# Kernel tuning notes

Measured on AMD Instinct MI355X. Metric: run time of the kernel, lower is better.

Reference implementation:

```python
import jax, jax.numpy as jnp
import numpy as np

KERNEL_MUL = 2.0
KERNEL_NUM = 5


def setup_inputs() -> dict:
    key = jax.random.key(0)
    k1, k2 = jax.random.split(key)
    N, D = 4096, 256
    source = jax.random.normal(k1, (N, D), dtype=jnp.float32)
    target = jax.random.normal(k2, (N, D), dtype=jnp.float32)
    return {"source": source, "target": target}


def _gaussian_kernel_sum(source, target):
    # total: [2N, D]
    total = jnp.concatenate([source, target], axis=0)
    n = total.shape[0]
    sq = jnp.sum(total * total, axis=1)  # [2N]
    L2 = sq[:, None] + sq[None, :] - 2.0 * (total @ total.T)  # [2N, 2N]
    # Bandwidth from detached mean of off-diagonal-normalized sum (torch uses .data)
    bandwidth = jax.lax.stop_gradient(jnp.sum(L2)) / (n * n - n)
    bandwidth = bandwidth / (KERNEL_MUL ** (KERNEL_NUM // 2))
    kernels = sum(
        jnp.exp(-L2 / (bandwidth * (KERNEL_MUL ** i))) for i in range(KERNEL_NUM)
    )
    return kernels


def reference(source, target):
    b = source.shape[0]
    K = _gaussian_kernel_sum(source, target)
    XX = jnp.mean(K[:b, :b])
    YY = jnp.mean(K[b:, b:])
    XY = jnp.mean(K[:b, b:])
    YX = jnp.mean(K[b:, :b])
    return XX + YY - XY - YX
```

## Files before the change

kernel.cpp:

```cpp
#include <hip/hip_runtime.h>


#define NROWS 8192
#define HALF  4096
#define DIM   256
#define CONVB 256
#define NTILE 2080

typedef __bf16 bf16x8 __attribute__((ext_vector_type(8)));
typedef float f32x4 __attribute__((ext_vector_type(4)));
typedef unsigned short ushort8 __attribute__((ext_vector_type(8)));

__device__ __forceinline__ const float* row_ptr(const float* src, const float* tgt, int r) {
    return (r < HALF) ? (src + (size_t)r * DIM) : (tgt + (size_t)(r - HALF) * DIM);
}

__device__ __forceinline__ unsigned short bf16_rne(float x) {
    unsigned int u = __builtin_bit_cast(unsigned int, x);
    return (unsigned short)((u + 0x7FFFu + ((u >> 16) & 1u)) >> 16);
}

__global__ __launch_bounds__(256) void k_conv(const float* __restrict__ src,
                                              const float* __restrict__ tgt,
                                              unsigned short* __restrict__ hi,
                                              float* __restrict__ sq,
                                              float* __restrict__ part,
                                              double* __restrict__ parts1,
                                              float* __restrict__ out) {
    __shared__ __align__(16) unsigned short sh_hi[32 * 32 * 8];
    __shared__ float4 cs[4][64];
    __shared__ double s1s[4];

    int w = threadIdx.x >> 6, lane = threadIdx.x & 63;
    int r0 = blockIdx.x * 32;
    int g  = lane >> 1, j = lane & 1;

    float4 v[8];
    #pragma unroll
    for (int i = 0; i < 8; ++i) {
        int row = r0 + w * 8 + i;
        v[i] = ((const float4*)row_ptr(src, tgt, row))[lane];
    }

    float4 csum = {0.f, 0.f, 0.f, 0.f};
    double s1w = 0.0;
    #pragma unroll
    for (int i = 0; i < 8; ++i) {
        int rl  = w * 8 + i;
        float xs[4] = {v[i].x, v[i].y, v[i].z, v[i].w};
        unsigned short hs[4];
        #pragma unroll
        for (int k = 0; k < 4; ++k) hs[k] = bf16_rne(xs[k]);
        ushort4 h4 = {hs[0], hs[1], hs[2], hs[3]};
        int so = (g * 32 + rl) * 8 + j * 4;
        *(ushort4*)&sh_hi[so] = h4;
        csum.x += xs[0]; csum.y += xs[1]; csum.z += xs[2]; csum.w += xs[3];
        float s = xs[0] * xs[0] + xs[1] * xs[1] + xs[2] * xs[2] + xs[3] * xs[3];
        #pragma unroll
        for (int off = 32; off; off >>= 1) s += __shfl_xor(s, off, 64);
        if (lane == 0) { sq[r0 + rl] = s; s1w += (double)s; }
    }
    __syncthreads();
    int panel = blockIdx.x >> 2, quarter = blockIdx.x & 3;
    #pragma unroll
    for (int c = threadIdx.x; c < 1024; c += 256) {
        int gg = c >> 5, r = c & 31;
        size_t goff = (((size_t)panel * 32 + gg) * 128 + quarter * 32 + r) * 8;
        *(ushort8*)&hi[goff] = *(const ushort8*)&sh_hi[c * 8];
    }
    cs[w][lane] = csum;
    if (lane == 0) s1s[w] = s1w;
    __syncthreads();
    if (w == 0) {
        float4 a = cs[0][lane], b = cs[1][lane], c = cs[2][lane], d = cs[3][lane];
        float4 tot = {a.x + b.x + c.x + d.x, a.y + b.y + c.y + d.y,
                      a.z + b.z + c.z + d.z, a.w + b.w + c.w + d.w};
        *(float4*)&part[(size_t)blockIdx.x * DIM + lane * 4] = tot;
        if (lane == 0) parts1[blockIdx.x] = s1s[0] + s1s[1] + s1s[2] + s1s[3];
    }
    if (blockIdx.x == 0 && threadIdx.x == 0) out[0] = 0.0f;
}

__global__ __launch_bounds__(256) void k_scale(const double* __restrict__ parts1,
                                               const float* __restrict__ part,
                                               float* __restrict__ scale) {
    __shared__ double sh[256];
    int t = threadIdx.x;
    sh[t] = parts1[t];
    __syncthreads();
    for (int off = 128; off; off >>= 1) {
        if (t < off) sh[t] += sh[t + off];
        __syncthreads();
    }
    double S1 = sh[0];
    __syncthreads();
    float c0 = 0.f, c1 = 0.f, c2 = 0.f, c3 = 0.f;
    #pragma unroll 16
    for (int b = 0; b < CONVB; b += 4) {
        c0 += part[(b + 0) * DIM + t];
        c1 += part[(b + 1) * DIM + t];
        c2 += part[(b + 2) * DIM + t];
        c3 += part[(b + 3) * DIM + t];
    }
    double c = (double)((c0 + c1) + (c2 + c3));
    sh[t] = c * c;
    __syncthreads();
    for (int off = 128; off; off >>= 1) {
        if (t < off) sh[t] += sh[t + off];
        __syncthreads();
    }
    if (t == 0) {
        double S2    = sh[0];
        double n     = (double)NROWS;
        double sumL2 = 2.0 * n * S1 - 2.0 * S2;
        double bw    = sumL2 / (n * n - n) / 4.0;
        *scale = (float)(-1.0 / (16.0 * bw * 0.69314718055994530942));
    }
}

__global__ __launch_bounds__(256, 2) void k_pairs(const unsigned short* __restrict__ hi,
                                                  const float* __restrict__ sq,
                                                  const float* __restrict__ scale_p,
                                                  float* __restrict__ out) {
    int id = blockIdx.x;
    int I = 0;
    for (;;) {
        int cnt = 64 - I;
        if (id < cnt) break;
        id -= cnt; ++I;
    }
    int J = I + id;

    __shared__ float wsum[4];

    int t    = threadIdx.x;
    int lane = t & 63;
    int w    = t >> 6;
    int lr   = lane & 15, lq = lane >> 4;
    int wr   = w >> 1, wc = w & 1;

    float wgt = (J == I) ? 1.0f : 2.0f;
    float sgn = ((I < 32) == (J < 32)) ? 1.0f : -1.0f;

    size_t aBase = (size_t)I * 4096 + (size_t)lq * 128 + wr * 64 + lr;
    size_t bBase = (size_t)J * 4096 + (size_t)lq * 128 + wc * 64 + lr;
    const ushort8* pAh = (const ushort8*)hi + aBase;
    const ushort8* pBh = (const ushort8*)hi + bBase;

    f32x4 acc[4][4];
    #pragma unroll
    for (int m = 0; m < 4; ++m)
        #pragma unroll
        for (int n = 0; n < 4; ++n) acc[m][n] = (f32x4){0.f, 0.f, 0.f, 0.f};

    bf16x8 aH[2][4], bH[2][4];
    #pragma unroll
    for (int m = 0; m < 4; ++m) aH[0][m] = __builtin_bit_cast(bf16x8, pAh[m * 16]);
    #pragma unroll
    for (int n = 0; n < 4; ++n) bH[0][n] = __builtin_bit_cast(bf16x8, pBh[n * 16]);

    #pragma unroll
    for (int it = 0; it < DIM / 32; ++it) {
        int cur = it & 1, nxt = cur ^ 1;
        if (it < DIM / 32 - 1) {
            #pragma unroll
            for (int m = 0; m < 4; ++m)
                aH[nxt][m] = __builtin_bit_cast(bf16x8, pAh[(it + 1) * 512 + m * 16]);
            #pragma unroll
            for (int n = 0; n < 4; ++n)
                bH[nxt][n] = __builtin_bit_cast(bf16x8, pBh[(it + 1) * 512 + n * 16]);
        }
        #pragma unroll
        for (int m = 0; m < 4; ++m)
            #pragma unroll
            for (int n = 0; n < 4; ++n)
                acc[m][n] = __builtin_amdgcn_mfma_f32_16x16x32_bf16(aH[cur][m], bH[cur][n], acc[m][n], 0, 0, 0);
    }

    float scale = *scale_p;
    int ro_eff = I * 128 + wr * 64;
    int co_eff = J * 128 + wc * 64;
    float4 sqa4[4];
    float  sqbv[4];
    #pragma unroll
    for (int m = 0; m < 4; ++m) sqa4[m] = *(const float4*)&sq[ro_eff + m * 16 + lq * 4];
    #pragma unroll
    for (int n = 0; n < 4; ++n) sqbv[n] = sq[co_eff + n * 16 + lr];

    float tsum = 0.0f;
    #pragma unroll
    for (int m = 0; m < 4; ++m) {
        float sa[4] = {sqa4[m].x, sqa4[m].y, sqa4[m].z, sqa4[m].w};
        #pragma unroll
        for (int n = 0; n < 4; ++n) {
            #pragma unroll
            for (int r = 0; r < 4; ++r) {
                float L2  = sa[r] + sqbv[n] - 2.0f * acc[m][n][r];
                float u   = __builtin_amdgcn_exp2f(scale * L2);
                float u2  = u * u;
                float u4  = u2 * u2;
                float u8  = u4 * u4;
                float u16 = u8 * u8;
                tsum += u + u2 + u4 + u8 + u16;
            }
        }
    }

    #pragma unroll
    for (int off = 32; off; off >>= 1) tsum += __shfl_xor(tsum, off, 64);
    if (lane == 0) wsum[w] = tsum;
    __syncthreads();
    if (t == 0) {
        float tot = wsum[0] + wsum[1] + wsum[2] + wsum[3];
        atomicAdd(out, tot * sgn * wgt * (1.0f / ((float)HALF * (float)HALF)));
    }
}

extern "C" void kernel_launch(void* const* d_in, const int* in_sizes, int n_in,
                              void* d_out, int out_size, void* d_ws, size_t ws_size,
                              hipStream_t stream) {
    const float* src = (const float*)d_in[0];
    const float* tgt = (const float*)d_in[1];
    float* out = (float*)d_out;

    char* ws = (char*)d_ws;
    float*  scale  = (float*)(ws + 16);
    float*  sq     = (float*)(ws + 64);
    float*  part   = (float*)(ws + 64 + 32768);
    double* parts1 = (double*)(ws + 64 + 32768 + 262144);
    unsigned short* hi = (unsigned short*)(ws + 297024);

    k_conv <<<CONVB, 256, 0, stream>>>(src, tgt, hi, sq, part, parts1, out);
    k_scale<<<1, 256, 0, stream>>>(parts1, part, scale);
    k_pairs<<<NTILE, 256, 0, stream>>>(hi, sq, scale, out);
}
```

Before: 111.0 us.

## Switch Gram matrix computation from bf16 to fp8 MFMA with fp8-consistent norms

Operands are now quantized to fp8 (e4m3) instead of bf16, and the pairwise dot products use the fp8 16x16x32 MFMA. Row squared norms used in the L2 formula are computed from the dequantized fp8 values so that the diagonal stays near zero, while the bandwidth statistic still uses exact fp32 norms. The packed layout is reorganised into 16-byte chunks holding two k-slices, and all operand fragments are loaded up front instead of double-buffered. This halves the operand bytes read per tile and uses a higher-throughput MFMA, at the cost of a large precision loss in the dot products that may push the result outside tolerance.

```diff
diff --git a/kernel.cpp b/kernel.cpp
--- a/kernel.cpp
+++ b/kernel.cpp
@@ -7,33 +7,25 @@
 #define CONVB 256
 #define NTILE 2080
 
-typedef __bf16 bf16x8 __attribute__((ext_vector_type(8)));
 typedef float f32x4 __attribute__((ext_vector_type(4)));
-typedef unsigned short ushort8 __attribute__((ext_vector_type(8)));
 
 __device__ __forceinline__ const float* row_ptr(const float* src, const float* tgt, int r) {
     return (r < HALF) ? (src + (size_t)r * DIM) : (tgt + (size_t)(r - HALF) * DIM);
 }
 
-__device__ __forceinline__ unsigned short bf16_rne(float x) {
-    unsigned int u = __builtin_bit_cast(unsigned int, x);
-    return (unsigned short)((u + 0x7FFFu + ((u >> 16) & 1u)) >> 16);
-}
-
 __global__ __launch_bounds__(256) void k_conv(const float* __restrict__ src,
                                               const float* __restrict__ tgt,
-                                              unsigned short* __restrict__ hi,
+                                              unsigned char* __restrict__ hi,
                                               float* __restrict__ sq,
                                               float* __restrict__ part,
                                               double* __restrict__ parts1,
                                               float* __restrict__ out) {
-    __shared__ __align__(16) unsigned short sh_hi[32 * 32 * 8];
+    __shared__ __align__(16) unsigned char sh8[32 * 256];
     __shared__ float4 cs[4][64];
     __shared__ double s1s[4];
 
     int w = threadIdx.x >> 6, lane = threadIdx.x & 63;
     int r0 = blockIdx.x * 32;
-    int g  = lane >> 1, j = lane & 1;
 
     float4 v[8];
     #pragma unroll
@@ -48,25 +40,39 @@
     for (int i = 0; i < 8; ++i) {
         int rl  = w * 8 + i;
         float xs[4] = {v[i].x, v[i].y, v[i].z, v[i].w};
-        unsigned short hs[4];
-        #pragma unroll
-        for (int k = 0; k < 4; ++k) hs[k] = bf16_rne(xs[k]);
-        ushort4 h4 = {hs[0], hs[1], hs[2], hs[3]};
-        int so = (g * 32 + rl) * 8 + j * 4;
-        *(ushort4*)&sh_hi[so] = h4;
+        int pk = __builtin_amdgcn_cvt_pk_fp8_f32(xs[0], xs[1], 0, false);
+        pk     = __builtin_amdgcn_cvt_pk_fp8_f32(xs[2], xs[3], pk, true);
+        int o  = lane >> 1, h = lane & 1;
+        *(int*)&sh8[rl * 256 + (((o ^ rl) & 31) << 3) + (h << 2)] = pk;
         csum.x += xs[0]; csum.y += xs[1]; csum.z += xs[2]; csum.w += xs[3];
-        float s = xs[0] * xs[0] + xs[1] * xs[1] + xs[2] * xs[2] + xs[3] * xs[3];
-        #pragma unroll
-        for (int off = 32; off; off >>= 1) s += __shfl_xor(s, off, 64);
-        if (lane == 0) { sq[r0 + rl] = s; s1w += (double)s; }
+        float sf = xs[0]*xs[0] + xs[1]*xs[1] + xs[2]*xs[2] + xs[3]*xs[3];
+        float q0 = __builtin_amdgcn_cvt_f32_fp8(pk, 0);
+        float q1 = __builtin_amdgcn_cvt_f32_fp8(pk, 1);
+        float q2 = __builtin_amdgcn_cvt_f32_fp8(pk, 2);
+        float q3 = __builtin_amdgcn_cvt_f32_fp8(pk, 3);
+        float sQ = q0*q0 + q1*q1 + q2*q2 + q3*q3;
+        #pragma unroll
+        for (int off = 32; off; off >>= 1) {
+            sf += __shfl_xor(sf, off, 64);
+            sQ += __shfl_xor(sQ, off, 64);
+        }
+        if (lane == 0) { sq[r0 + rl] = sQ; s1w += (double)sf; }
     }
     __syncthreads();
     int panel = blockIdx.x >> 2, quarter = blockIdx.x & 3;
     #pragma unroll
-    for (int c = threadIdx.x; c < 1024; c += 256) {
-        int gg = c >> 5, r = c & 31;
-        size_t goff = (((size_t)panel * 32 + gg) * 128 + quarter * 32 + r) * 8;
-        *(ushort8*)&hi[goff] = *(const ushort8*)&sh_hi[c * 8];
+    for (int c = threadIdx.x; c < 512; c += 256) {
+        int u = c >> 5, rl = c & 31;
+        int tt = u >> 2, j = u & 3;
+        int o0 = 8 * tt + j;
+        int o1 = 8 * tt + 4 + j;
+        unsigned long long q0 = *(const unsigned long long*)
+            &sh8[rl * 256 + (((o0 ^ rl) & 31) << 3)];
+        unsigned long long q1 = *(const unsigned long long*)
+            &sh8[rl * 256 + (((o1 ^ rl) & 31) << 3)];
+        ulonglong2 q = {q0, q1};
+        size_t goff = ((size_t)panel * 2048 + (size_t)u * 128 + quarter * 32 + rl);
+        ((ulonglong2*)hi)[goff] = q;
     }
     cs[w][lane] = csum;
     if (lane == 0) s1s[w] = s1w;
@@ -118,7 +124,7 @@
     }
 }
 
-__global__ __launch_bounds__(256, 2) void k_pairs(const unsigned short* __restrict__ hi,
+__global__ __launch_bounds__(256, 2) void k_pairs(const unsigned char* __restrict__ hi,
                                                   const float* __restrict__ sq,
                                                   const float* __restrict__ scale_p,
                                                   float* __restrict__ out) {
@@ -142,10 +148,9 @@
     float wgt = (J == I) ? 1.0f : 2.0f;
     float sgn = ((I < 32) == (J < 32)) ? 1.0f : -1.0f;
 
-    size_t aBase = (size_t)I * 4096 + (size_t)lq * 128 + wr * 64 + lr;
-    size_t bBase = (size_t)J * 4096 + (size_t)lq * 128 + wc * 64 + lr;
-    const ushort8* pAh = (const ushort8*)hi + aBase;
-    const ushort8* pBh = (const ushort8*)hi + bBase;
+    const ulonglong2* hp = (const ulonglong2*)hi;
+    const ulonglong2* pA = hp + (size_t)I * 2048 + (size_t)lq * 128 + wr * 64 + lr;
+    const ulonglong2* pB = hp + (size_t)J * 2048 + (size_t)lq * 128 + wc * 64 + lr;
 
     f32x4 acc[4][4];
     #pragma unroll
@@ -153,28 +158,29 @@
         #pragma unroll
         for (int n = 0; n < 4; ++n) acc[m][n] = (f32x4){0.f, 0.f, 0.f, 0.f};
 
-    bf16x8 aH[2][4], bH[2][4];
-    #pragma unroll
-    for (int m = 0; m < 4; ++m) aH[0][m] = __builtin_bit_cast(bf16x8, pAh[m * 16]);
-    #pragma unroll
-    for (int n = 0; n < 4; ++n) bH[0][n] = __builtin_bit_cast(bf16x8, pBh[n * 16]);
-
-    #pragma unroll
-    for (int it = 0; it < DIM / 32; ++it) {
-        int cur = it & 1, nxt = cur ^ 1;
-        if (it < DIM / 32 - 1) {
-            #pragma unroll
-            for (int m = 0; m < 4; ++m)
-                aH[nxt][m] = __builtin_bit_cast(bf16x8, pAh[(it + 1) * 512 + m * 16]);
-            #pragma unroll
-            for (int n = 0; n < 4; ++n)
-                bH[nxt][n] = __builtin_bit_cast(bf16x8, pBh[(it + 1) * 512 + n * 16]);
-        }
+    ulonglong2 fA[4][4], fB[4][4];
+    #pragma unroll
+    for (int tt = 0; tt < 4; ++tt) {
+        #pragma unroll
+        for (int m = 0; m < 4; ++m) fA[tt][m] = pA[tt * 512 + m * 16];
+        #pragma unroll
+        for (int n = 0; n < 4; ++n) fB[tt][n] = pB[tt * 512 + n * 16];
+    }
+
+    #pragma unroll
+    for (int tt = 0; tt < 4; ++tt) {
         #pragma unroll
         for (int m = 0; m < 4; ++m)
             #pragma unroll
             for (int n = 0; n < 4; ++n)
-                acc[m][n] = __builtin_amdgcn_mfma_f32_16x16x32_bf16(aH[cur][m], bH[cur][n], acc[m][n], 0, 0, 0);
+                acc[m][n] = __builtin_amdgcn_mfma_f32_16x16x32_fp8_fp8(
+                    (long)fA[tt][m].x, (long)fB[tt][n].x, acc[m][n], 0, 0, 0);
+        #pragma unroll
+        for (int m = 0; m < 4; ++m)
+            #pragma unroll
+            for (int n = 0; n < 4; ++n)
+                acc[m][n] = __builtin_amdgcn_mfma_f32_16x16x32_fp8_fp8(
+                    (long)fA[tt][m].y, (long)fB[tt][n].y, acc[m][n], 0, 0, 0);
     }
 
     float scale = *scale_p;
@@ -228,7 +234,7 @@
     float*  sq     = (float*)(ws + 64);
     float*  part   = (float*)(ws + 64 + 32768);
     double* parts1 = (double*)(ws + 64 + 32768 + 262144);
-    unsigned short* hi = (unsigned short*)(ws + 297024);
+    unsigned char* hi = (unsigned char*)(ws + 297024);
 
     k_conv <<<CONVB, 256, 0, stream>>>(src, tgt, hi, sq, part, parts1, out);
     k_scale<<<1, 256, 0, stream>>>(parts1, part, scale);
```

Result: faster. 104.6 us (-5.8%).
